# Kernel tuning notes

Measured on AMD Instinct MI355X. Metric: run time of the kernel, lower is better.

Reference implementation:

```python
import jax, jax.numpy as jnp
import numpy as np

EMB = 2048
N_HEADS = 16
HEAD_DIM = EMB // N_HEADS
ROPE_BASE = 10000.0


def _rope_cos_sin(seq_len, head_dim, dtype):
    inv_freq = 1.0 / (ROPE_BASE ** (jnp.arange(0, head_dim, 2, dtype=jnp.float32) / head_dim))
    t = jnp.arange(seq_len, dtype=jnp.float32)
    freqs = jnp.einsum('s,d->sd', t, inv_freq)          # [S, head_dim/2]
    emb = jnp.concatenate([freqs, freqs], axis=-1)       # [S, head_dim]
    return jnp.cos(emb).astype(dtype), jnp.sin(emb).astype(dtype)


def _rotate_half(x):
    x1, x2 = jnp.split(x, 2, axis=-1)
    return jnp.concatenate([-x2, x1], axis=-1)


def _apply_rope(x, cos, sin):
    # x: [B, H, S, D]; cos/sin: [S, D]
    return x * cos[None, None, :, :] + _rotate_half(x) * sin[None, None, :, :]


def setup_inputs() -> dict:
    key = jax.random.key(0)
    k1, k2, k3 = jax.random.split(key, 3)
    B, S = 4, 2048
    x = jax.random.normal(k1, (B, S, EMB), dtype=jnp.float32)
    # Additive causal mask: 0 on/below diagonal, -1e9 above.
    causal = jnp.triu(jnp.full((S, S), -1e9, dtype=jnp.float32), k=1)
    att_mask = causal[None, None, :, :]
    Wqkv = jax.random.normal(k2, (3 * EMB, EMB), dtype=jnp.float32) * (EMB ** -0.5)
    Wout = jax.random.normal(k3, (EMB, EMB), dtype=jnp.float32) * (EMB ** -0.5)
    return {"x": x, "att_mask": att_mask, "Wqkv": Wqkv, "Wout": Wout}


def reference(x, att_mask, Wqkv, Wout):
    B, S, E = x.shape
    qkv = jnp.einsum('bse,fe->bsf', x, Wqkv)             # [B, S, 3E]
    q, k, v = jnp.split(qkv, 3, axis=-1)
    def to_heads(t):
        return t.reshape(B, S, N_HEADS, HEAD_DIM).transpose(0, 2, 1, 3)  # [B,H,S,D]
    q, k, v = to_heads(q), to_heads(k), to_heads(v)
    cos, sin = _rope_cos_sin(S, HEAD_DIM, x.dtype)
    q = _apply_rope(q, cos, sin)
    k = _apply_rope(k, cos, sin)
    scaling = HEAD_DIM ** -0.5
    dots = jnp.einsum('bhqd,bhkd->bhqk', q, k) * scaling
    dots = dots + att_mask
    attn = jax.nn.softmax(dots, axis=-1)
    out = jnp.einsum('bhqk,bhkd->bhqd', attn, v)         # [B,H,S,D]
    out = out.transpose(0, 2, 1, 3).reshape(B, S, E)
    return jnp.einsum('bse,fe->bsf', out, Wout)
```

## Files before the change

kernel.cpp:

```cpp
#include <hip/hip_runtime.h>
#include <stdint.h>

typedef __attribute__((ext_vector_type(8))) short short8_t;
typedef __attribute__((ext_vector_type(4))) float f32x4;
typedef __attribute__((ext_vector_type(16))) float f32x16;

__device__ __forceinline__ short f2bf(float f) {
  union { float f; uint32_t u; } v; v.f = f;
  uint32_t r = v.u + 0x7FFFu + ((v.u >> 16) & 1u);
  return (short)(r >> 16);
}
__device__ __forceinline__ float bf2f(short s) {
  union { uint32_t u; float f; } v; v.u = ((uint32_t)(uint16_t)s) << 16; return v.f;
}
__device__ __forceinline__ void gld16(const void* g, void* l) {
  __builtin_amdgcn_global_load_lds((const __attribute__((address_space(1))) void*)g,
                                   (__attribute__((address_space(3))) void*)l, 16, 0, 0);
}

__global__ __launch_bounds__(256) void conv_kernel(const float* __restrict__ in,
                                                   short* __restrict__ out, int n4) {
  int i = blockIdx.x * 256 + threadIdx.x;
  const int stride = gridDim.x * 256;
  for (; i < n4; i += stride) {
    float4 v = reinterpret_cast<const float4*>(in)[i];
    short4 o;
    o.x = f2bf(v.x); o.y = f2bf(v.y); o.z = f2bf(v.z); o.w = f2bf(v.w);
    reinterpret_cast<short4*>(out)[i] = o;
  }
}

__device__ __forceinline__ void storeC(float* C, size_t i, float v) { C[i] = v; }
__device__ __forceinline__ void storeC(short* C, size_t i, float v) { C[i] = f2bf(v); }

template <typename OT, bool FUSEV>
__global__ __launch_bounds__(512, 2) void gemm32(const short* __restrict__ A,
                                                 const short* __restrict__ B,
                                                 OT* __restrict__ C,
                                                 short* __restrict__ VT,
                                                 int M, int N, int K) {
  __shared__ __align__(16) short lds[65536];
  const int tid = threadIdx.x, lane = tid & 63, w = tid >> 6;
  const int wr = w >> 2, wc = w & 3;
  const int l31 = lane & 31, hl = lane >> 5;
  const int xcd = (int)blockIdx.x & 7;
  const int t = (int)blockIdx.x >> 3;
  const int bx = (t & 7) + 8 * (t >> 5);
  const int by = xcd * 4 + ((t >> 3) & 3);
  const size_t m0 = (size_t)by * 256, n0 = (size_t)bx * 256;
  const size_t Kb = (size_t)K * 2;
  const char* aqp = (const char*)A + (m0 + w * 32 + l31) * Kb + hl * 16;
  const char* bqp = (const char*)B + (n0 + w * 32 + l31) * Kb + hl * 16;
  char* alds = (char*)lds;
  const int aoff = wr * 16384 + lane * 16;
  const int boff = 65536 + wc * 8192 + lane * 16;
  f32x16 acc[4][2] = {};
  const int NT = K >> 6, NIT = NT >> 1;

  short8_t a0, a1, a2, a3, b0, b1, c0, c1, c2, c3, d0, d1;

#define RD_A(reg, IMM) \
  asm volatile("ds_read_b128 %0, %1 offset:%c2" : "=v"(reg) : "v"(aoff), "i"(IMM))
#define RD_B(reg, IMM) \
  asm volatile("ds_read_b128 %0, %1 offset:%c2" : "=v"(reg) : "v"(boff), "i"(IMM))

#define MFMA8(A0, A1, A2, A3, B0, B1)                                          \
  acc[0][0] = __builtin_amdgcn_mfma_f32_32x32x16_bf16(A0, B0, acc[0][0], 0, 0, 0); \
  acc[0][1] = __builtin_amdgcn_mfma_f32_32x32x16_bf16(A0, B1, acc[0][1], 0, 0, 0); \
  acc[1][0] = __builtin_amdgcn_mfma_f32_32x32x16_bf16(A1, B0, acc[1][0], 0, 0, 0); \
  acc[1][1] = __builtin_amdgcn_mfma_f32_32x32x16_bf16(A1, B1, acc[1][1], 0, 0, 0); \
  acc[2][0] = __builtin_amdgcn_mfma_f32_32x32x16_bf16(A2, B0, acc[2][0], 0, 0, 0); \
  acc[2][1] = __builtin_amdgcn_mfma_f32_32x32x16_bf16(A2, B1, acc[2][1], 0, 0, 0); \
  acc[3][0] = __builtin_amdgcn_mfma_f32_32x32x16_bf16(A3, B0, acc[3][0], 0, 0, 0); \
  acc[3][1] = __builtin_amdgcn_mfma_f32_32x32x16_bf16(A3, B1, acc[3][1], 0, 0, 0)

  gld16(aqp + 0, alds + ((w * 4 + 0) << 10));
  gld16(aqp + 32, alds + ((w * 4 + 1) << 10));
  gld16(bqp + 0, alds + 65536 + ((w * 4 + 0) << 10));
  gld16(bqp + 32, alds + 65536 + ((w * 4 + 1) << 10));
  gld16(aqp + 64, alds + ((w * 4 + 2) << 10));
  gld16(aqp + 96, alds + ((w * 4 + 3) << 10));
  gld16(bqp + 64, alds + 65536 + ((w * 4 + 2) << 10));
  gld16(bqp + 96, alds + 65536 + ((w * 4 + 3) << 10));

#define PH(KSL, CB, PT)                                                          \
  asm volatile("s_waitcnt vmcnt(4)" ::: "memory");                               \
  asm volatile("s_barrier" ::: "memory");                                        \
  RD_A(a0, (CB) + 0 * 4096 + (KSL) * 1024);                                      \
  RD_A(a1, (CB) + 1 * 4096 + (KSL) * 1024);                                      \
  RD_A(a2, (CB) + 2 * 4096 + (KSL) * 1024);                                      \
  RD_A(a3, (CB) + 3 * 4096 + (KSL) * 1024);                                      \
  RD_B(b0, (CB) + 0 * 4096 + (KSL) * 1024);                                      \
  RD_B(b1, (CB) + 1 * 4096 + (KSL) * 1024);                                      \
  RD_A(c0, (CB) + 0 * 4096 + ((KSL) + 1) * 1024);                                \
  RD_A(c1, (CB) + 1 * 4096 + ((KSL) + 1) * 1024);                                \
  RD_A(c2, (CB) + 2 * 4096 + ((KSL) + 1) * 1024);                                \
  RD_A(c3, (CB) + 3 * 4096 + ((KSL) + 1) * 1024);                                \
  RD_B(d0, (CB) + 0 * 4096 + ((KSL) + 1) * 1024);                                \
  RD_B(d1, (CB) + 1 * 4096 + ((KSL) + 1) * 1024);                                \
  gld16(aqp + (PT) + (KSL) * 32, alds + ((CB) ^ 32768) + ((w * 4 + (KSL)) << 10));       \
  gld16(aqp + (PT) + ((KSL) + 1) * 32, alds + ((CB) ^ 32768) + ((w * 4 + (KSL) + 1) << 10)); \
  gld16(bqp + (PT) + (KSL) * 32, alds + 65536 + ((CB) ^ 32768) + ((w * 4 + (KSL)) << 10));   \
  gld16(bqp + (PT) + ((KSL) + 1) * 32, alds + 65536 + ((CB) ^ 32768) + ((w * 4 + (KSL) + 1) << 10)); \
  asm volatile("s_waitcnt lgkmcnt(6)" ::: "memory");                             \
  __builtin_amdgcn_sched_barrier(0);                                             \
  __builtin_amdgcn_s_setprio(1);                                                 \
  MFMA8(a0, a1, a2, a3, b0, b1);                                                 \
  __builtin_amdgcn_s_setprio(0);                                                 \
  asm volatile("s_waitcnt lgkmcnt(0)" ::: "memory");                             \
  __builtin_amdgcn_sched_barrier(0);                                             \
  __builtin_amdgcn_s_setprio(1);                                                 \
  MFMA8(c0, c1, c2, c3, d0, d1);                                                 \
  __builtin_amdgcn_s_setprio(0)

  for (int it = 0; it < NIT; ++it) {
    const int T = it << 1;
    const int p1 = (T + 1) << 7;
    const int p2 = (T + 2 < NT ? T + 2 : NT - 1) << 7;
    PH(0, 0, p1);
    PH(2, 0, p1);
    PH(0, 32768, p2);
    PH(2, 32768, p2);
  }
#undef PH
#undef MFMA8
#undef RD_A
#undef RD_B

#pragma unroll
  for (int m = 0; m < 4; ++m)
#pragma unroll
    for (int n = 0; n < 2; ++n) {
      const size_t col = n0 + wc * 64 + n * 32 + l31;
      const int rbase = (int)m0 + wr * 128 + m * 32 + hl * 4;
      bool tovt = false;
      if constexpr (FUSEV) tovt = (col >= 4096);
      if (tovt) {
        const size_t cc = col - 4096;
        const size_t bb = (size_t)(rbase >> 11);
#pragma unroll
        for (int j = 0; j < 4; ++j) {
          const int s0 = (rbase & 2047) + j * 8;
          short4 o;
          o.x = f2bf(acc[m][n][j * 4 + 0]);
          o.y = f2bf(acc[m][n][j * 4 + 1]);
          o.z = f2bf(acc[m][n][j * 4 + 2]);
          o.w = f2bf(acc[m][n][j * 4 + 3]);
          *(short4*)&VT[(bb * 2048 + cc) * 2048 + s0] = o;
        }
      } else {
#pragma unroll
        for (int j = 0; j < 4; ++j)
#pragma unroll
          for (int r = 0; r < 4; ++r)
            storeC(C, (size_t)(rbase + j * 8 + r) * (size_t)N + col, acc[m][n][j * 4 + r]);
      }
    }
}

__global__ __launch_bounds__(256) void rope_kernel(short* __restrict__ qkv) {
  const int g = blockIdx.x * 256 + threadIdx.x;
  const int jg = g & 7;
  const int h = (g >> 3) & 15;
  const int bs = g >> 7;
  const int s = bs & 2047;
  const size_t base = (size_t)bs * 6144 + 2048 + h * 128 + jg * 8;
  short8_t lo = *(short8_t*)&qkv[base];
  short8_t hi = *(short8_t*)&qkv[base + 64];
  short8_t olo, ohi;
#pragma unroll
  for (int t = 0; t < 8; ++t) {
    const int j = jg * 8 + t;
    const float inv = exp2f((float)j * -0.20762050593046f);
    float sn, cn;
    sincosf((float)s * inv, &sn, &cn);
    const float a = bf2f(lo[t]), b = bf2f(hi[t]);
    olo[t] = f2bf(a * cn - b * sn);
    ohi[t] = f2bf(b * cn + a * sn);
  }
  *(short8_t*)&qkv[base] = olo;
  *(short8_t*)&qkv[base + 64] = ohi;
}

__global__ __launch_bounds__(256) void attn_kernel(const short* __restrict__ qkv,
                                                   const short* __restrict__ vt,
                                                   short* __restrict__ o) {
  __shared__ __align__(16) short Kl[2][64 * 128];
  __shared__ __align__(16) short Vl[2][128 * 64];
  __shared__ __align__(16) short Pl[4][16 * 72];
  const int tid = threadIdx.x, lane = tid & 63, w = tid >> 6;
  const int c = lane & 15, g4 = lane >> 4;
  const int blk = blockIdx.x;
  const int xcd = blk & 7;
  const int l = blk >> 3;
  const int bh = xcd * 8 + (l >> 5);
  const int h = bh & 15, b = bh >> 4;
  const int q0 = (31 - (l & 31)) * 64;
  const int srow = q0 + w * 16 + c;

  short8_t qf[4];
  {
    const size_t qr = ((size_t)b * 2048 + srow) * 6144 + h * 128;
    float fl[4][8];
#pragma unroll
    for (int dc = 0; dc < 4; ++dc) {
      short8_t rawv = *(const short8_t*)&qkv[qr + dc * 32 + g4 * 8];
#pragma unroll
      for (int t = 0; t < 8; ++t) fl[dc][t] = bf2f(rawv[t]);
    }
#pragma unroll
    for (int pd = 0; pd < 2; ++pd)
#pragma unroll
      for (int t = 0; t < 8; ++t) {
        const int j = pd * 32 + g4 * 8 + t;
        const float inv = exp2f((float)j * -0.20762050593046f);
        float sn, cn;
        sincosf((float)srow * inv, &sn, &cn);
        const float a = fl[pd][t], bb = fl[pd + 2][t];
        fl[pd][t] = a * cn - bb * sn;
        fl[pd + 2][t] = bb * cn + a * sn;
      }
#pragma unroll
    for (int dc = 0; dc < 4; ++dc) {
      short8_t q8;
#pragma unroll
      for (int t = 0; t < 8; ++t) q8[t] = f2bf(fl[dc][t]);
      qf[dc] = q8;
    }
  }

  f32x4 acc_o[8] = {};
  float rs[4] = {0.f, 0.f, 0.f, 0.f};
  const float scale2 = 0.12751875222364685f;
  const char* Kbase = (const char*)qkv + ((size_t)b * 2048 * 6144 + 2048 + h * 128) * 2;
  const char* Vbase = (const char*)vt + ((size_t)(b * 16 + h) * 128 * 2048) * 2;

  const char* kq[4];
  const char* vq[4];
#pragma unroll
  for (int i = 0; i < 4; ++i) {
    const int L = ((w * 4 + i) << 10) + lane * 16;
    {
      const int row = L >> 8, inner = L & 255;
      kq[i] = Kbase + (size_t)row * 12288 + (inner ^ ((row & 7) << 4));
    }
    {
      const int row = L >> 7, inner = L & 127;
      vq[i] = Vbase + (size_t)row * 4096 + (inner ^ ((row & 7) << 4));
    }
  }
  auto stage = [&](int buf, int kv0) {
#pragma unroll
    for (int i = 0; i < 4; ++i) {
      gld16(kq[i] + (size_t)kv0 * 12288, (char*)Kl + (buf << 14) + ((w * 4 + i) << 10));
      gld16(vq[i] + (size_t)kv0 * 2, (char*)Vl + (buf << 14) + ((w * 4 + i) << 10));
    }
  };

  stage(0, 0);
  __syncthreads();
  int cur = 0;
  for (int kv0 = 0; kv0 <= q0; kv0 += 64) {
    if (kv0 + 64 <= q0) stage(cur ^ 1, kv0 + 64);
    const char* Kb = (const char*)Kl + (cur << 14);
    const char* Vb = (const char*)Vl + (cur << 14);
    const bool diag = (kv0 == q0);
    float p[4][4];
#pragma unroll
    for (int kt = 0; kt < 4; ++kt) {
      f32x4 s4 = {};
      const int krow = kt * 16 + c;
      __builtin_amdgcn_s_setprio(1);
#pragma unroll
      for (int dc = 0; dc < 4; ++dc) {
        const int inner = (dc * 64 + g4 * 16) ^ ((krow & 7) << 4);
        short8_t kf = *(const short8_t*)(Kb + krow * 256 + inner);
        s4 = __builtin_amdgcn_mfma_f32_16x16x32_bf16(qf[dc], kf, s4, 0, 0, 0);
      }
      __builtin_amdgcn_s_setprio(0);
#pragma unroll
      for (int r = 0; r < 4; ++r) {
        float v = s4[r] * scale2 - 8.0f;
        if (diag) {
          const int kc = kv0 + kt * 16 + c;
          const int qr2 = q0 + w * 16 + g4 * 4 + r;
          if (kc > qr2) v = -1e30f;
        }
        const float pe = exp2f(v);
        p[kt][r] = pe;
        rs[r] += pe;
      }
    }
#pragma unroll
    for (int kt = 0; kt < 4; ++kt)
#pragma unroll
      for (int r = 0; r < 4; r += 2) {
        uint32_t pk;
        asm("v_cvt_pk_bf16_f32 %0, %1, %2" : "=v"(pk) : "v"(p[kt][r]), "v"(p[kt][r + 1]));
        Pl[w][(g4 * 4 + r) * 72 + kt * 16 + c] = (short)(pk & 0xffffu);
        Pl[w][(g4 * 4 + r + 1) * 72 + kt * 16 + c] = (short)(pk >> 16);
      }
#pragma unroll
    for (int kk = 0; kk < 2; ++kk) {
      short8_t pf = *(const short8_t*)&Pl[w][c * 72 + kk * 32 + g4 * 8];
      __builtin_amdgcn_s_setprio(1);
#pragma unroll
      for (int dt = 0; dt < 8; ++dt) {
        const int vrow = dt * 16 + c;
        const int inner = (kk * 64 + g4 * 16) ^ ((vrow & 7) << 4);
        short8_t vf = *(const short8_t*)(Vb + vrow * 128 + inner);
        acc_o[dt] = __builtin_amdgcn_mfma_f32_16x16x32_bf16(pf, vf, acc_o[dt], 0, 0, 0);
      }
      __builtin_amdgcn_s_setprio(0);
    }
    __syncthreads();
    cur ^= 1;
  }
#pragma unroll
  for (int off = 1; off < 16; off <<= 1)
#pragma unroll
    for (int r = 0; r < 4; ++r) rs[r] += __shfl_xor(rs[r], off);
  const size_t ob = ((size_t)b * 2048 + q0 + w * 16 + g4 * 4) * 2048 + h * 128;
#pragma unroll
  for (int dt = 0; dt < 8; ++dt)
#pragma unroll
    for (int r = 0; r < 4; ++r)
      o[ob + (size_t)r * 2048 + dt * 16 + c] = f2bf(acc_o[dt][r] / rs[r]);
}

extern "C" void kernel_launch(void* const* d_in, const int* in_sizes, int n_in,
                              void* d_out, int out_size, void* d_ws, size_t ws_size,
                              hipStream_t stream) {
  const float* x = (const float*)d_in[0];
  const float* Wqkv = (const float*)d_in[2];
  const float* Wout = (const float*)d_in[3];
  float* out = (float*)d_out;
  char* ws = (char*)d_ws;
  short* xb   = (short*)ws;
  short* wqb  = (short*)(ws + 33554432ull);
  short* qkv  = (short*)(ws + 58720256ull);
  short* vt   = (short*)(ws + 159383552ull);
  short* attno = xb;
  short* woutb = wqb;

  conv_kernel<<<2048, 256, 0, stream>>>(x, xb, 16777216 / 4);
  conv_kernel<<<2048, 256, 0, stream>>>(Wqkv, wqb, 12582912 / 4);
  gemm32<short, true><<<768, 512, 0, stream>>>(xb, wqb, qkv, vt, 8192, 6144, 2048);
  conv_kernel<<<2048, 256, 0, stream>>>(Wout, woutb, 4194304 / 4);
  rope_kernel<<<4096, 256, 0, stream>>>(qkv);
  attn_kernel<<<2048, 256, 0, stream>>>(qkv, vt, attno);
  gemm32<float, false><<<256, 512, 0, stream>>>(attno, woutb, out, nullptr, 8192, 2048, 2048);
}
```

Before: 529.9 us.

## Restructure GEMM to 4 waves with 128x128 per-wave tiles and register double-buffering

The GEMM kernel drops from 8 waves per 256x256 block to 4, so each wave now computes a 128x128 sub-tile (4x4 MFMA accumulators) instead of 128x64. Each wave stages two rows' worth of global-to-LDS loads, and LDS fragment reads are double-buffered in registers so the next k-slice is read while the current MFMAs run. The aim is higher arithmetic intensity per LDS read and better overlap of LDS reads with MFMA. The cost is far more accumulator registers (256 floats per lane) and fewer waves per CU (launch bounds 256,1), which may reduce latency hiding.

```diff
diff --git a/kernel.cpp b/kernel.cpp
--- a/kernel.cpp
+++ b/kernel.cpp
@@ -34,14 +34,14 @@
 __device__ __forceinline__ void storeC(short* C, size_t i, float v) { C[i] = f2bf(v); }
 
 template <typename OT, bool FUSEV>
-__global__ __launch_bounds__(512, 2) void gemm32(const short* __restrict__ A,
+__global__ __launch_bounds__(256, 1) void gemm32(const short* __restrict__ A,
                                                  const short* __restrict__ B,
                                                  OT* __restrict__ C,
                                                  short* __restrict__ VT,
                                                  int M, int N, int K) {
   __shared__ __align__(16) short lds[65536];
   const int tid = threadIdx.x, lane = tid & 63, w = tid >> 6;
-  const int wr = w >> 2, wc = w & 3;
+  const int wr = w >> 1, wc = w & 1;
   const int l31 = lane & 31, hl = lane >> 5;
   const int xcd = (int)blockIdx.x & 7;
   const int t = (int)blockIdx.x >> 3;
@@ -49,89 +49,97 @@
   const int by = xcd * 4 + ((t >> 3) & 3);
   const size_t m0 = (size_t)by * 256, n0 = (size_t)bx * 256;
   const size_t Kb = (size_t)K * 2;
-  const char* aqp = (const char*)A + (m0 + w * 32 + l31) * Kb + hl * 16;
-  const char* bqp = (const char*)B + (n0 + w * 32 + l31) * Kb + hl * 16;
+  const char* sa[2];
+  const char* sb[2];
+#pragma unroll
+  for (int i = 0; i < 2; ++i) {
+    const size_t row = (size_t)((2 * w + i) * 32 + l31);
+    sa[i] = (const char*)A + (m0 + row) * Kb + hl * 16;
+    sb[i] = (const char*)B + (n0 + row) * Kb + hl * 16;
+  }
   char* alds = (char*)lds;
   const int aoff = wr * 16384 + lane * 16;
-  const int boff = 65536 + wc * 8192 + lane * 16;
-  f32x16 acc[4][2] = {};
+  const int boff = 65536 + wc * 16384 + lane * 16;
+  f32x16 acc[4][4] = {};
   const int NT = K >> 6, NIT = NT >> 1;
 
-  short8_t a0, a1, a2, a3, b0, b1, c0, c1, c2, c3, d0, d1;
-
-#define RD_A(reg, IMM) \
-  asm volatile("ds_read_b128 %0, %1 offset:%c2" : "=v"(reg) : "v"(aoff), "i"(IMM))
-#define RD_B(reg, IMM) \
-  asm volatile("ds_read_b128 %0, %1 offset:%c2" : "=v"(reg) : "v"(boff), "i"(IMM))
-
-#define MFMA8(A0, A1, A2, A3, B0, B1)                                          \
-  acc[0][0] = __builtin_amdgcn_mfma_f32_32x32x16_bf16(A0, B0, acc[0][0], 0, 0, 0); \
-  acc[0][1] = __builtin_amdgcn_mfma_f32_32x32x16_bf16(A0, B1, acc[0][1], 0, 0, 0); \
-  acc[1][0] = __builtin_amdgcn_mfma_f32_32x32x16_bf16(A1, B0, acc[1][0], 0, 0, 0); \
-  acc[1][1] = __builtin_amdgcn_mfma_f32_32x32x16_bf16(A1, B1, acc[1][1], 0, 0, 0); \
-  acc[2][0] = __builtin_amdgcn_mfma_f32_32x32x16_bf16(A2, B0, acc[2][0], 0, 0, 0); \
-  acc[2][1] = __builtin_amdgcn_mfma_f32_32x32x16_bf16(A2, B1, acc[2][1], 0, 0, 0); \
-  acc[3][0] = __builtin_amdgcn_mfma_f32_32x32x16_bf16(A3, B0, acc[3][0], 0, 0, 0); \
-  acc[3][1] = __builtin_amdgcn_mfma_f32_32x32x16_bf16(A3, B1, acc[3][1], 0, 0, 0)
-
-  gld16(aqp + 0, alds + ((w * 4 + 0) << 10));
-  gld16(aqp + 32, alds + ((w * 4 + 1) << 10));
-  gld16(bqp + 0, alds + 65536 + ((w * 4 + 0) << 10));
-  gld16(bqp + 32, alds + 65536 + ((w * 4 + 1) << 10));
-  gld16(aqp + 64, alds + ((w * 4 + 2) << 10));
-  gld16(aqp + 96, alds + ((w * 4 + 3) << 10));
-  gld16(bqp + 64, alds + 65536 + ((w * 4 + 2) << 10));
-  gld16(bqp + 96, alds + 65536 + ((w * 4 + 3) << 10));
-
-#define PH(KSL, CB, PT)                                                          \
-  asm volatile("s_waitcnt vmcnt(4)" ::: "memory");                               \
-  asm volatile("s_barrier" ::: "memory");                                        \
-  RD_A(a0, (CB) + 0 * 4096 + (KSL) * 1024);                                      \
-  RD_A(a1, (CB) + 1 * 4096 + (KSL) * 1024);                                      \
-  RD_A(a2, (CB) + 2 * 4096 + (KSL) * 1024);                                      \
-  RD_A(a3, (CB) + 3 * 4096 + (KSL) * 1024);                                      \
-  RD_B(b0, (CB) + 0 * 4096 + (KSL) * 1024);                                      \
-  RD_B(b1, (CB) + 1 * 4096 + (KSL) * 1024);                                      \
-  RD_A(c0, (CB) + 0 * 4096 + ((KSL) + 1) * 1024);                                \
-  RD_A(c1, (CB) + 1 * 4096 + ((KSL) + 1) * 1024);                                \
-  RD_A(c2, (CB) + 2 * 4096 + ((KSL) + 1) * 1024);                                \
-  RD_A(c3, (CB) + 3 * 4096 + ((KSL) + 1) * 1024);                                \
-  RD_B(d0, (CB) + 0 * 4096 + ((KSL) + 1) * 1024);                                \
-  RD_B(d1, (CB) + 1 * 4096 + ((KSL) + 1) * 1024);                                \
-  gld16(aqp + (PT) + (KSL) * 32, alds + ((CB) ^ 32768) + ((w * 4 + (KSL)) << 10));       \
-  gld16(aqp + (PT) + ((KSL) + 1) * 32, alds + ((CB) ^ 32768) + ((w * 4 + (KSL) + 1) << 10)); \
-  gld16(bqp + (PT) + (KSL) * 32, alds + 65536 + ((CB) ^ 32768) + ((w * 4 + (KSL)) << 10));   \
-  gld16(bqp + (PT) + ((KSL) + 1) * 32, alds + 65536 + ((CB) ^ 32768) + ((w * 4 + (KSL) + 1) << 10)); \
-  asm volatile("s_waitcnt lgkmcnt(6)" ::: "memory");                             \
-  __builtin_amdgcn_sched_barrier(0);                                             \
-  __builtin_amdgcn_s_setprio(1);                                                 \
-  MFMA8(a0, a1, a2, a3, b0, b1);                                                 \
-  __builtin_amdgcn_s_setprio(0);                                                 \
-  asm volatile("s_waitcnt lgkmcnt(0)" ::: "memory");                             \
-  __builtin_amdgcn_sched_barrier(0);                                             \
-  __builtin_amdgcn_s_setprio(1);                                                 \
-  MFMA8(c0, c1, c2, c3, d0, d1);                                                 \
+  short8_t af[2][4], bf_[2][4];
+
+#define STAGE_SLICE(KS, CBN, TOFF)                                                     \
+  gld16(sa[0] + (TOFF) + (KS) * 32, alds + (CBN) + ((2 * w + 0) << 12) + ((KS) << 10)); \
+  gld16(sa[1] + (TOFF) + (KS) * 32, alds + (CBN) + ((2 * w + 1) << 12) + ((KS) << 10)); \
+  gld16(sb[0] + (TOFF) + (KS) * 32,                                                     \
+        alds + 65536 + (CBN) + ((2 * w + 0) << 12) + ((KS) << 10));                     \
+  gld16(sb[1] + (TOFF) + (KS) * 32,                                                     \
+        alds + 65536 + (CBN) + ((2 * w + 1) << 12) + ((KS) << 10))
+
+#define RD8(S, CB, KS)                                                                   \
+  asm volatile("ds_read_b128 %0, %1 offset:%c2" : "=v"(af[S][0]) : "v"(aoff),            \
+               "i"((CB) + 0 * 4096 + (KS) * 1024));                                      \
+  asm volatile("ds_read_b128 %0, %1 offset:%c2" : "=v"(af[S][1]) : "v"(aoff),            \
+               "i"((CB) + 1 * 4096 + (KS) * 1024));                                      \
+  asm volatile("ds_read_b128 %0, %1 offset:%c2" : "=v"(af[S][2]) : "v"(aoff),            \
+               "i"((CB) + 2 * 4096 + (KS) * 1024));                                      \
+  asm volatile("ds_read_b128 %0, %1 offset:%c2" : "=v"(af[S][3]) : "v"(aoff),            \
+               "i"((CB) + 3 * 4096 + (KS) * 1024));                                      \
+  asm volatile("ds_read_b128 %0, %1 offset:%c2" : "=v"(bf_[S][0]) : "v"(boff),           \
+               "i"((CB) + 0 * 4096 + (KS) * 1024));                                      \
+  asm volatile("ds_read_b128 %0, %1 offset:%c2" : "=v"(bf_[S][1]) : "v"(boff),           \
+               "i"((CB) + 1 * 4096 + (KS) * 1024));                                      \
+  asm volatile("ds_read_b128 %0, %1 offset:%c2" : "=v"(bf_[S][2]) : "v"(boff),           \
+               "i"((CB) + 2 * 4096 + (KS) * 1024));                                      \
+  asm volatile("ds_read_b128 %0, %1 offset:%c2" : "=v"(bf_[S][3]) : "v"(boff),           \
+               "i"((CB) + 3 * 4096 + (KS) * 1024))
+
+#define MFMA16(S)                                                                        \
+  __builtin_amdgcn_s_setprio(1);                                                         \
+  _Pragma("unroll") for (int mi = 0; mi < 4; ++mi) {                                     \
+    _Pragma("unroll") for (int ni = 0; ni < 4; ++ni)                                     \
+      acc[mi][ni] = __builtin_amdgcn_mfma_f32_32x32x16_bf16(af[S][mi], bf_[S][ni],       \
+                                                            acc[mi][ni], 0, 0, 0);       \
+  }                                                                                      \
   __builtin_amdgcn_s_setprio(0)
+
+#define PH(S, CB, KS, RCB, RKS, SCBN, SKS, TOFF)                   \
+  asm volatile("s_waitcnt vmcnt(8)" ::: "memory");                 \
+  asm volatile("s_barrier" ::: "memory");                          \
+  RD8(S ^ 1, RCB, RKS);                                            \
+  STAGE_SLICE(SKS, SCBN, TOFF);                                    \
+  asm volatile("s_waitcnt lgkmcnt(8)" ::: "memory");               \
+  __builtin_amdgcn_sched_barrier(0);                               \
+  MFMA16(S)
+
+  STAGE_SLICE(0, 0, 0);
+  STAGE_SLICE(1, 0, 0);
+  STAGE_SLICE(2, 0, 0);
+  STAGE_SLICE(3, 0, 0);
+  asm volatile("s_waitcnt vmcnt(12)" ::: "memory");
+  asm volatile("s_barrier" ::: "memory");
+  RD8(0, 0, 0);
 
   for (int it = 0; it < NIT; ++it) {
     const int T = it << 1;
-    const int p1 = (T + 1) << 7;
-    const int p2 = (T + 2 < NT ? T + 2 : NT - 1) << 7;
-    PH(0, 0, p1);
-    PH(2, 0, p1);
-    PH(0, 32768, p2);
-    PH(2, 32768, p2);
+    const int t1 = (T + 1) << 7;
+    const int t2 = (T + 2 < NT ? T + 2 : NT - 1) << 7;
+    PH(0, 0, 0,     0, 1,     32768, 0, t1);
+    PH(1, 0, 1,     0, 2,     32768, 1, t1);
+    PH(0, 0, 2,     0, 3,     32768, 2, t1);
+    PH(1, 0, 3,     32768, 0, 32768, 3, t1);
+    PH(0, 32768, 0, 32768, 1, 0, 0, t2);
+    PH(1, 32768, 1, 32768, 2, 0, 1, t2);
+    PH(0, 32768, 2, 32768, 3, 0, 2, t2);
+    PH(1, 32768, 3, 0, 0,     0, 3, t2);
   }
 #undef PH
-#undef MFMA8
-#undef RD_A
-#undef RD_B
+#undef MFMA16
+#undef RD8
+#undef STAGE_SLICE
 
 #pragma unroll
   for (int m = 0; m < 4; ++m)
 #pragma unroll
-    for (int n = 0; n < 2; ++n) {
-      const size_t col = n0 + wc * 64 + n * 32 + l31;
+    for (int n = 0; n < 4; ++n) {
+      const size_t col = n0 + wc * 128 + n * 32 + l31;
       const int rbase = (int)m0 + wr * 128 + m * 32 + hl * 4;
       bool tovt = false;
       if constexpr (FUSEV) tovt = (col >= 4096);
@@ -345,9 +353,9 @@
 
   conv_kernel<<<2048, 256, 0, stream>>>(x, xb, 16777216 / 4);
   conv_kernel<<<2048, 256, 0, stream>>>(Wqkv, wqb, 12582912 / 4);
-  gemm32<short, true><<<768, 512, 0, stream>>>(xb, wqb, qkv, vt, 8192, 6144, 2048);
+  gemm32<short, true><<<768, 256, 0, stream>>>(xb, wqb, qkv, vt, 8192, 6144, 2048);
   conv_kernel<<<2048, 256, 0, stream>>>(Wout, woutb, 4194304 / 4);
   rope_kernel<<<4096, 256, 0, stream>>>(qkv);
   attn_kernel<<<2048, 256, 0, stream>>>(qkv, vt, attno);
-  gemm32<float, false><<<256, 512, 0, stream>>>(attno, woutb, out, nullptr, 8192, 2048, 2048);
-}
+  gemm32<float, false><<<256, 256, 0, stream>>>(attno, woutb, out, nullptr, 8192, 2048, 2048);
+}
```

Result: slower. 577.2 us (+8.9%).
